# Kernel tuning notes

Measured on AMD Instinct MI355X. Metric: run time of the kernel, lower is better.

## Reference

```python
import jax, jax.numpy as jnp
import numpy as np

N_EMB = 8192
EMB_DIM = 128
BETA = 0.25


def setup_inputs() -> dict:
    key = jax.random.key(0)
    k1, k2 = jax.random.split(key)
    x = jax.random.normal(k1, (32, EMB_DIM, 1024), dtype=jnp.float32)
    embeddings = jax.random.normal(k2, (N_EMB, EMB_DIM), dtype=jnp.float32)
    return {"x": x, "embeddings": embeddings}


def reference(x, embeddings):
    # preprocess: swap chn_dim(=1) with last dim, flatten to tokens
    xt = jnp.swapaxes(x, 1, -1)                      # [B, L, D]
    flat = xt.reshape(-1, EMB_DIM)                   # [N, D]
    prenorm = jnp.linalg.norm(flat - jnp.mean(flat)) / np.sqrt(float(flat.size))

    # squared-euclidean distances via matmul + norms: [N, n_emb]
    s1 = jnp.sum(flat * flat, axis=1, keepdims=True)
    s2 = jnp.sum(embeddings * embeddings, axis=1)
    sim = flat @ embeddings.T
    distances = s1 + s2 - 2.0 * sim

    min_distance = jnp.min(distances, axis=1)
    idx = jnp.argmin(distances, axis=1)              # [N] int
    fit = jnp.mean(jnp.nan_to_num(min_distance))

    # EMA scatter statistics (one-hot matmul in torch == segment_sum here)
    k_sum = jax.ops.segment_sum(flat, idx, num_segments=N_EMB)         # [n_emb, D]
    k_elem = jax.ops.segment_sum(jnp.ones_like(idx, jnp.float32), idx,
                                 num_segments=N_EMB)                   # [n_emb]
    k_prob = k_elem / jnp.sum(k_elem)
    entropy = -jnp.sum(k_prob * jnp.log(k_prob + 1e-8))

    # embedding gather, reshape back to channels-first
    quantized = embeddings[idx].reshape(xt.shape)    # [B, L, D]
    quantized = jnp.swapaxes(quantized, 1, -1)       # [B, D, L]

    # ema_update=True -> codebook_loss = 0, only commit loss
    commit_loss = BETA * jnp.mean((jax.lax.stop_gradient(quantized) - x) ** 2)
    loss = commit_loss

    # straight-through estimator
    out = x + jax.lax.stop_gradient(quantized - x)
    return out, quantized, loss, fit, prenorm, entropy, k_sum, k_elem
```

## Files before the change

kernel.cpp:

```cpp
#include <hip/hip_runtime.h>
#include <math.h>
#include <float.h>

#define BB 32
#define DD 128
#define LL 1024
#define NN 32768
#define NE 8192
#define XSZ 4194304
#define OUT_OFF_Q     4194304
#define OUT_OFF_SCAL  8388608
#define OUT_OFF_KSUM  8388612
#define OUT_OFF_KELEM 9437188

typedef unsigned int u32;
typedef unsigned short u16;
typedef int   i32x4 __attribute__((ext_vector_type(4)));
typedef float f32x4 __attribute__((ext_vector_type(4)));

__device__ inline float waveSum(float v){
  #pragma unroll
  for (int o = 32; o > 0; o >>= 1) v += __shfl_down(v, o, 64);
  return v;
}
__device__ inline double waveSumD(double v){
  #pragma unroll
  for (int o = 32; o > 0; o >>= 1) v += __shfl_down(v, o, 64);
  return v;
}

__global__ __launch_bounds__(256) void prep_kernel(const float* __restrict__ e,
    u16* __restrict__ eh8, int* __restrict__ s2seed,
    int* __restrict__ cnt, float* __restrict__ accs)
{
  int t = threadIdx.x;
  if (blockIdx.x < 32) cnt[blockIdx.x * 256 + t] = 0;
  if (blockIdx.x == 32 && t < 16) accs[t] = 0.f;

  int row = blockIdx.x * 4 + (t >> 6);
  int kd  = t & 63;
  float2 ev = *reinterpret_cast<const float2*>(&e[row * DD + kd * 2]);
  int e0 = __float2int_rn(ev.x * 4096.f);
  int e1 = __float2int_rn(ev.y * 4096.f);
  e0 = min(max(e0, -32639), 32639);
  e1 = min(max(e1, -32639), 32639);
  double sq = (double)e0 * (double)e0 + (double)e1 * (double)e1;
  sq = waveSumD(sq);
  if (kd == 0){
    int sd = (int)(sq * (1.0 / 131072.0));
    sd = min(sd, 120000);
    s2seed[row] = -sd;
  }
  int h0 = (e0 + 128) >> 8;
  int h1 = (e1 + 128) >> 8;
  int k = kd * 2;
  int T16 = row >> 4, lr = row & 15;
  int kt2 = k >> 6, lg = (k >> 4) & 3, j = k & 15;
  int du16 = (((T16*2 + kt2) * 1024) + lg*256 + lr*16 + j) >> 1;
  eh8[du16] = (u16)((h0 & 255) | ((h1 & 255) << 8));
}

#define LOADSET(AH0,AH1,SEED,TT) \
  { int T_ = (TT); \
    AH0 = *(const i32x4*)(ehp + (size_t)(T_*2 + 0) * 256); \
    AH1 = *(const i32x4*)(ehp + (size_t)(T_*2 + 1) * 256); \
    SEED = s2s4[T_*4 + sofs]; }

#define MFMA2S(SLOT, CT, AH0,AH1,SEED) \
  SLOT = __builtin_amdgcn_mfma_i32_16x16x64_i8(AH0, Bh[CT][0], SEED, 0,0,0); \
  SLOT = __builtin_amdgcn_mfma_i32_16x16x64_i8(AH1, Bh[CT][1], SLOT, 0,0,0);

#define KEYS1(T1V, CT, JV) \
  { _Pragma("unroll") \
    for (int r = 0; r < 4; ++r){ \
      int key = (int)(((u32)T1V[r] << 13) + (u32)(JV[r])); \
      int k2n; \
      asm("v_med3_i32 %0, %1, %2, %3" \
          : "=v"(k2n) : "v"(key), "v"(k1[CT]), "v"(k2[CT])); \
      k2[CT] = k2n; \
      k1[CT] = max(key, k1[CT]); \
    } }

#define TILE_BODY(AH0,AH1,SEED,JV) \
  MFMA2S(sa, 0, AH0,AH1,SEED) \
  MFMA2S(sb, 1, AH0,AH1,SEED) \
  KEYS1(sa, 0, JV) \
  MFMA2S(sa, 2, AH0,AH1,SEED) \
  KEYS1(sb, 1, JV) \
  MFMA2S(sb, 3, AH0,AH1,SEED) \
  KEYS1(sa, 2, JV) \
  KEYS1(sb, 3, JV)

__global__ __launch_bounds__(256, 4) void argmin_mfma(
    const float* __restrict__ x,
    const u32* __restrict__ eh8,
    const i32x4* __restrict__ s2s4,
    int* __restrict__ idx1o, int* __restrict__ idx2o)
{
  __shared__ int kk1[1024];
  __shared__ int kk2[1024];

  int t  = threadIdx.x;
  int w  = t >> 6;
  int l  = t & 63;
  int lr = l & 15;
  int lg = l >> 4;

  int blk  = blockIdx.x;
  int half = blk >> 9;
  int tb   = blk & 511;
  int hb64 = half * 64;

  int n0 = tb * 64;
  int b  = n0 >> 10;
  int l0 = n0 & 1023;
  const float* xb = x + (size_t)b * (DD * LL);

  i32x4 Bh[4][2];
  #pragma unroll
  for (int ct = 0; ct < 4; ++ct){
    int tok = l0 + ct*16 + lr;
    #pragma unroll
    for (int kt = 0; kt < 2; ++kt){
      #pragma unroll
      for (int dw = 0; dw < 4; ++dw){
        u32 hw = 0;
        #pragma unroll
        for (int bb = 0; bb < 4; ++bb){
          int k = kt*64 + lg*16 + dw*4 + bb;
          int xi = __float2int_rn(xb[(size_t)k * LL + tok] * 4096.f);
          xi = min(max(xi, -32639), 32639);
          int h  = (xi + 128) >> 8;
          hw |= ((u32)h & 255u) << (8*bb);
        }
        Bh[ct][kt][dw] = (int)hw;
      }
    }
  }

  int k1[4], k2[4];
  #pragma unroll
  for (int ct = 0; ct < 4; ++ct){ k1[ct] = (int)0x80000000; k2[ct] = (int)0x80000000; }

  int jvA[4], jvB[4];
  #pragma unroll
  for (int r = 0; r < 4; ++r){
    jvA[r] = 8191 - (hb64*64 + w*16 + lg*4 + r);
    jvB[r] = jvA[r] - 64;
  }

  const u32* ehp = eh8 + (size_t)l * 4;
  int sofs = lg;

  i32x4 Ah0A, Ah1A, seedA;
  i32x4 Ah0B, Ah1B, seedB;
  i32x4 sa, sb;

  LOADSET(Ah0A, Ah1A, seedA, (hb64 + 0)*4 + w)
  LOADSET(Ah0B, Ah1B, seedB, (hb64 + 1)*4 + w)

  for (int it = 0; it < 64; it += 2){
    TILE_BODY(Ah0A, Ah1A, seedA, jvA)
    if (it + 2 < 64){
      LOADSET(Ah0A, Ah1A, seedA, (hb64 + it + 2)*4 + w)
    }
    #pragma unroll
    for (int r = 0; r < 4; ++r) jvA[r] -= 128;

    TILE_BODY(Ah0B, Ah1B, seedB, jvB)
    if (it + 3 < 64){
      LOADSET(Ah0B, Ah1B, seedB, (hb64 + it + 3)*4 + w)
    }
    #pragma unroll
    for (int r = 0; r < 4; ++r) jvB[r] -= 128;
  }

  #pragma unroll
  for (int ct = 0; ct < 4; ++ct){
    int sidx = (ct*16 + lr)*16 + w*4 + lg;
    kk1[sidx] = k1[ct];
    kk2[sidx] = k2[ct];
  }
  __syncthreads();
  if (t < 64){
    int K1 = (int)0x80000000, K2 = (int)0x80000000;
    #pragma unroll 4
    for (int s = 0; s < 16; ++s){
      int a = kk1[t*16 + s], b2 = kk2[t*16 + s];
      int mn = min(a, K1);  K2 = max(mn, K2);  K1 = max(a, K1);
      mn = min(b2, K1);     K2 = max(mn, K2);  K1 = max(b2, K1);
    }
    idx1o[half*NN + n0 + t] = 8191 - (K1 & 8191);
    idx2o[half*NN + n0 + t] = 8191 - (K2 & 8191);
  }
}

__global__ __launch_bounds__(128) void fixup_kernel(const float* __restrict__ x,
    const float* __restrict__ e,
    const int* __restrict__ idx1, const int* __restrict__ idx2,
    int* __restrict__ idxf, int* __restrict__ cnt, float* __restrict__ accs,
    float* __restrict__ out, float* __restrict__ quant)
{
  int n = blockIdx.x * 128 + threadIdx.x;
  int b = n >> 10, l = n & 1023;
  size_t xoff = (size_t)b * (DD * LL) + l;
  const float* xb = x + xoff;
  int js[4];
  js[0] = idx1[n];      js[1] = idx2[n];
  js[2] = idx1[NN + n]; js[3] = idx2[NN + n];
  const float4* er[4];
  #pragma unroll
  for (int i = 0; i < 4; ++i) er[i] = (const float4*)&e[js[i] * DD];

  float s1 = 0.f, sx = 0.f;
  float dt[4] = {0.f,0.f,0.f,0.f}, sq[4] = {0.f,0.f,0.f,0.f};
  #pragma unroll 2
  for (int k4 = 0; k4 < 32; ++k4){
    float xv[4];
    #pragma unroll
    for (int r = 0; r < 4; ++r) xv[r] = xb[(size_t)(k4*4 + r) * LL];
    s1 = fmaf(xv[0],xv[0], fmaf(xv[1],xv[1], fmaf(xv[2],xv[2], fmaf(xv[3],xv[3], s1))));
    sx += xv[0] + xv[1] + xv[2] + xv[3];
    #pragma unroll
    for (int i = 0; i < 4; ++i){
      float4 v = er[i][k4];
      dt[i] = fmaf(xv[0],v.x, fmaf(xv[1],v.y, fmaf(xv[2],v.z, fmaf(xv[3],v.w, dt[i]))));
      sq[i] = fmaf(v.x,v.x, fmaf(v.y,v.y, fmaf(v.z,v.z, fmaf(v.w,v.w, sq[i]))));
    }
  }
  int jw = js[0];
  float dw = s1 + sq[0] - 2.f * dt[0];
  #pragma unroll
  for (int i = 1; i < 4; ++i){
    float di = s1 + sq[i] - 2.f * dt[i];
    if (di < dw || (di == dw && js[i] < jw)) { dw = di; jw = js[i]; }
  }
  idxf[n] = jw;
  atomicAdd(&cnt[jw], 1);

  const float4* ew = (const float4*)&e[jw * DD];
  #pragma unroll 2
  for (int k4 = 0; k4 < 32; ++k4){
    float4 q = ew[k4];
    #pragma unroll
    for (int r = 0; r < 4; ++r){
      size_t o = xoff + (size_t)(k4*4 + r) * LL;
      float qr = (r == 0) ? q.x : (r == 1) ? q.y : (r == 2) ? q.z : q.w;
      out[o]   = qr;
      quant[o] = qr;
    }
  }
  dw = waveSum(dw); s1 = waveSum(s1); sx = waveSum(sx);
  if ((threadIdx.x & 63) == 0){
    atomicAdd(&accs[3], dw);
    atomicAdd(&accs[1], s1);
    atomicAdd(&accs[0], sx);
  }
}

__global__ __launch_bounds__(1024) void prefix_kernel(const int* __restrict__ cnt,
    int* __restrict__ cursor, float* __restrict__ kelem,
    const float* __restrict__ accs, float* __restrict__ scal)
{
  __shared__ int sc[1024];
  __shared__ double er[16];
  int t = threadIdx.x;
  int c[8]; int s = 0;
  #pragma unroll
  for (int i = 0; i < 8; ++i){ c[i] = cnt[t*8 + i]; s += c[i]; }
  sc[t] = s;
  __syncthreads();
  for (int off = 1; off < 1024; off <<= 1){
    int v = sc[t];
    int u = (t >= off) ? sc[t - off] : 0;
    __syncthreads();
    sc[t] = v + u;
    __syncthreads();
  }
  int base = t ? sc[t-1] : 0;
  #pragma unroll
  for (int i = 0; i < 8; ++i){
    cursor[t*8 + i] = base;
    kelem[t*8 + i] = (float)c[i];
    base += c[i];
  }
  double es = 0.0;
  #pragma unroll
  for (int i = 0; i < 8; ++i){
    float p = (float)c[i] * (1.0f / NN);
    es += (double)(p * logf(p + 1e-8f));
  }
  es = waveSumD(es);
  if ((t & 63) == 0) er[t >> 6] = es;
  __syncthreads();
  if (t == 0){
    double ent = 0.0;
    #pragma unroll
    for (int i = 0; i < 16; ++i) ent += er[i];
    ent = -ent;
    float sum = accs[0], sq = accs[1], fitsum = accs[3];
    double mu  = (double)sum / (double)XSZ;
    double var = (double)sq / (double)XSZ - mu * mu;
    if (var < 0) var = 0;
    scal[0] = (float)(0.25 * (double)fitsum / (double)XSZ);
    scal[1] = (float)((double)fitsum / (double)NN);
    scal[2] = (float)sqrt(var);
    scal[3] = (float)ent;
  }
}

__global__ __launch_bounds__(256) void scatter_kernel(const int* __restrict__ idxf,
    int* __restrict__ cursor, int* __restrict__ order, int* __restrict__ jsorted)
{
  int n = blockIdx.x * 256 + threadIdx.x;
  int j = idxf[n];
  int p = atomicAdd(&cursor[j], 1);
  order[p] = n;
  jsorted[p] = j;
}

__global__ __launch_bounds__(256) void transpose_kernel(const float* __restrict__ x,
    float* __restrict__ xT, float* __restrict__ ksum)
{
  __shared__ float tile[64][137];
  int t = threadIdx.x;
  {
    const float4 z = make_float4(0.f,0.f,0.f,0.f);
    float4* kz = (float4*)&ksum[(size_t)blockIdx.x * 2048 + t * 8];
    kz[0] = z; kz[1] = z;
  }
  int b  = blockIdx.x >> 4;
  int l0 = (blockIdx.x & 15) << 6;
  const float* xb = x + (size_t)b * (DD * LL);
  #pragma unroll
  for (int rep = 0; rep < 32; ++rep){
    int idx = rep * 256 + t;
    int d = idx >> 6, ll = idx & 63;
    tile[ll][d] = xb[d * LL + l0 + ll];
  }
  __syncthreads();
  int n0 = (b << 10) + l0;
  #pragma unroll
  for (int rep = 0; rep < 8; ++rep){
    int idx = rep * 256 + t;
    int row = idx >> 5, c4 = idx & 31;
    float4 v;
    v.x = tile[row][c4*4+0]; v.y = tile[row][c4*4+1];
    v.z = tile[row][c4*4+2]; v.w = tile[row][c4*4+3];
    *(float4*)&xT[(size_t)(n0 + row) * DD + c4*4] = v;
  }
}

__global__ __launch_bounds__(256) void ksum_chunk_kernel(const float* __restrict__ xT,
    const int* __restrict__ order, const int* __restrict__ jsorted,
    float* __restrict__ ksum)
{
  int wv = threadIdx.x >> 6, lane = threadIdx.x & 63;
  int chunk = blockIdx.x * 4 + wv;
  int st = chunk * 32;
  int myo = order[st + (lane & 31)];
  int myj = jsorted[st + (lane & 31)];
  float a0 = 0.f, a1 = 0.f;
  bool inside = false;
  #pragma unroll
  for (int k = 0; k < 32; ++k){
    int j = __shfl(myj, k);
    int n = __shfl(myo, k);
    const float* xr = xT + (size_t)n * DD;
    a0 += xr[lane];
    a1 += xr[64 + lane];
    int jn = (k < 31) ? __shfl(myj, k + 1) : -1;
    if (jn != j){
      if (inside && k < 31){
        ksum[j * DD + lane]      = a0;
        ksum[j * DD + 64 + lane] = a1;
      } else {
        atomicAdd(&ksum[j * DD + lane], a0);
        atomicAdd(&ksum[j * DD + 64 + lane], a1);
      }
      a0 = 0.f; a1 = 0.f;
      inside = true;
    }
  }
}

__global__ __launch_bounds__(256) void ksum_kernel(const float* __restrict__ x,
    const int* __restrict__ order, const int* __restrict__ cnt,
    const int* __restrict__ cursor, float* __restrict__ ksum)
{
  int w = threadIdx.x >> 6, lane = threadIdx.x & 63;
  int j = blockIdx.x * 4 + w;
  int c = cnt[j];
  int st = cursor[j] - c;
  float a0 = 0.f, a1 = 0.f;
  for (int k = 0; k < c; ++k){
    int n = order[st + k];
    int b = n >> 10, l = n & 1023;
    const float* xb = x + (size_t)b * (DD * LL) + l;
    a0 += xb[lane * LL];
    a1 += xb[(lane + 64) * LL];
  }
  ksum[j * DD + lane]      = a0;
  ksum[j * DD + 64 + lane] = a1;
}

extern "C" void kernel_launch(void* const* d_in, const int* in_sizes, int n_in,
                              void* d_out, int out_size, void* d_ws, size_t ws_size,
                              hipStream_t stream)
{
  const float* x = (const float*)d_in[0];
  const float* e = (const float*)d_in[1];
  float* out   = (float*)d_out;
  float* quant = out + OUT_OFF_Q;
  float* scal  = out + OUT_OFF_SCAL;
  float* ksum  = out + OUT_OFF_KSUM;
  float* kelem = out + OUT_OFF_KELEM;

  char* wsb = (char*)d_ws;
  u16*   eh8     = (u16*)(wsb);
  int*   s2seed  = (int*)(wsb + 2097152);
  int*   idx1    = (int*)(wsb + 2129920);
  int*   idx2    = (int*)(wsb + 2392064);
  int*   idxf    = (int*)(wsb + 2654208);
  int*   cnt     = (int*)(wsb + 2785280);
  int*   cursor  = (int*)(wsb + 2818048);
  int*   order   = (int*)(wsb + 2850816);
  int*   jsorted = (int*)(wsb + 2981888);
  float* accs    = (float*)(wsb + 3112960);
  float* xT      = (float*)(wsb + 4194304);
  bool useXT = ws_size >= (size_t)(4194304 + 16777216);

  prep_kernel   <<<NE / 4,     256, 0, stream>>>(e, eh8, s2seed, cnt, accs);
  argmin_mfma   <<<1024,       256, 0, stream>>>(x, (const u32*)eh8,
                                                 (const i32x4*)s2seed, idx1, idx2);
  fixup_kernel  <<<NN / 128,   128, 0, stream>>>(x, e, idx1, idx2, idxf, cnt, accs,
                                                 out, quant);
  prefix_kernel <<<1,         1024, 0, stream>>>(cnt, cursor, kelem, accs, scal);
  scatter_kernel<<<NN / 256,   256, 0, stream>>>(idxf, cursor, order, jsorted);
  if (useXT){
    transpose_kernel <<<BB * 16, 256, 0, stream>>>(x, xT, ksum);
    ksum_chunk_kernel<<<NN / 128, 256, 0, stream>>>(xT, order, jsorted, ksum);
  } else {
    ksum_kernel      <<<NE / 4,  256, 0, stream>>>(x, order, cnt, cursor, ksum);
  }
}
```

Baseline: 147.6 us.

## Fuse x transpose into fixup kernel, split its D loop across waves, precompute codebook norms

The fixup kernel now runs 4 waves per 64 tokens. Each wave handles a quarter of the channel dimension, and partial dot products and norms are reduced through shared memory. It also writes the token-major copy of x that the separate transpose kernel used to build, so x is read once less. Codebook squared norms are computed once in prep instead of per candidate in fixup, and ksum zeroing moves into the scatter kernel. The ksum chunk size is halved to 16 to get more parallelism, at the cost of more atomics at chunk boundaries; the strided per-thread float4 xT writes may coalesce poorly.

After: 152.1 us. +3.1%, slower.

```diff
diff --git a/kernel.cpp b/kernel.cpp
--- a/kernel.cpp
+++ b/kernel.cpp
@@ -30,7 +30,7 @@
 }
 
 __global__ __launch_bounds__(256) void prep_kernel(const float* __restrict__ e,
-    u16* __restrict__ eh8, int* __restrict__ s2seed,
+    u16* __restrict__ eh8, int* __restrict__ s2seed, float* __restrict__ s2f,
     int* __restrict__ cnt, float* __restrict__ accs)
 {
   int t = threadIdx.x;
@@ -46,10 +46,13 @@
   e1 = min(max(e1, -32639), 32639);
   double sq = (double)e0 * (double)e0 + (double)e1 * (double)e1;
   sq = waveSumD(sq);
+  float sqf = ev.x * ev.x + ev.y * ev.y;
+  sqf = waveSum(sqf);
   if (kd == 0){
     int sd = (int)(sq * (1.0 / 131072.0));
     sd = min(sd, 120000);
     s2seed[row] = -sd;
+    s2f[row] = sqf;
   }
   int h0 = (e0 + 128) >> 8;
   int h1 = (e1 + 128) >> 8;
@@ -195,66 +198,93 @@
   }
 }
 
-__global__ __launch_bounds__(128) void fixup_kernel(const float* __restrict__ x,
-    const float* __restrict__ e,
+__global__ __launch_bounds__(256) void fixup_kernel(const float* __restrict__ x,
+    const float* __restrict__ e, const float* __restrict__ s2f,
     const int* __restrict__ idx1, const int* __restrict__ idx2,
     int* __restrict__ idxf, int* __restrict__ cnt, float* __restrict__ accs,
-    float* __restrict__ out, float* __restrict__ quant)
-{
-  int n = blockIdx.x * 128 + threadIdx.x;
-  int b = n >> 10, l = n & 1023;
-  size_t xoff = (size_t)b * (DD * LL) + l;
-  const float* xb = x + xoff;
+    float* __restrict__ out, float* __restrict__ quant, float* __restrict__ xT)
+{
+  __shared__ float red[5][4][64];
+  __shared__ int jws[64];
+
+  int t = threadIdx.x;
+  int w = t >> 6, l = t & 63;
+  int n0 = blockIdx.x * 64;
+  int n  = n0 + l;
+  int b  = n0 >> 10;
+  int l0 = n0 & 1023;
+  size_t base = (size_t)b * (DD * LL) + l0 + l;
+  const float* xb = x + base;
+
   int js[4];
   js[0] = idx1[n];      js[1] = idx2[n];
   js[2] = idx1[NN + n]; js[3] = idx2[NN + n];
-  const float4* er[4];
-  #pragma unroll
-  for (int i = 0; i < 4; ++i) er[i] = (const float4*)&e[js[i] * DD];
 
   float s1 = 0.f, sx = 0.f;
-  float dt[4] = {0.f,0.f,0.f,0.f}, sq[4] = {0.f,0.f,0.f,0.f};
-  #pragma unroll 2
-  for (int k4 = 0; k4 < 32; ++k4){
-    float xv[4];
-    #pragma unroll
-    for (int r = 0; r < 4; ++r) xv[r] = xb[(size_t)(k4*4 + r) * LL];
-    s1 = fmaf(xv[0],xv[0], fmaf(xv[1],xv[1], fmaf(xv[2],xv[2], fmaf(xv[3],xv[3], s1))));
-    sx += xv[0] + xv[1] + xv[2] + xv[3];
-    #pragma unroll
-    for (int i = 0; i < 4; ++i){
-      float4 v = er[i][k4];
-      dt[i] = fmaf(xv[0],v.x, fmaf(xv[1],v.y, fmaf(xv[2],v.z, fmaf(xv[3],v.w, dt[i]))));
-      sq[i] = fmaf(v.x,v.x, fmaf(v.y,v.y, fmaf(v.z,v.z, fmaf(v.w,v.w, sq[i]))));
-    }
-  }
-  int jw = js[0];
-  float dw = s1 + sq[0] - 2.f * dt[0];
-  #pragma unroll
-  for (int i = 1; i < 4; ++i){
-    float di = s1 + sq[i] - 2.f * dt[i];
-    if (di < dw || (di == dw && js[i] < jw)) { dw = di; jw = js[i]; }
-  }
-  idxf[n] = jw;
-  atomicAdd(&cnt[jw], 1);
-
-  const float4* ew = (const float4*)&e[jw * DD];
-  #pragma unroll 2
-  for (int k4 = 0; k4 < 32; ++k4){
-    float4 q = ew[k4];
-    #pragma unroll
-    for (int r = 0; r < 4; ++r){
-      size_t o = xoff + (size_t)(k4*4 + r) * LL;
-      float qr = (r == 0) ? q.x : (r == 1) ? q.y : (r == 2) ? q.z : q.w;
-      out[o]   = qr;
-      quant[o] = qr;
-    }
-  }
-  dw = waveSum(dw); s1 = waveSum(s1); sx = waveSum(sx);
-  if ((threadIdx.x & 63) == 0){
-    atomicAdd(&accs[3], dw);
-    atomicAdd(&accs[1], s1);
-    atomicAdd(&accs[0], sx);
+  float dt0 = 0.f, dt1 = 0.f, dt2 = 0.f, dt3 = 0.f;
+  int kbase = w * 32;
+  #pragma unroll
+  for (int k4 = 0; k4 < 8; ++k4){
+    int k = kbase + k4*4;
+    float x0 = xb[(size_t)(k+0) * LL];
+    float x1 = xb[(size_t)(k+1) * LL];
+    float x2 = xb[(size_t)(k+2) * LL];
+    float x3 = xb[(size_t)(k+3) * LL];
+    s1 = fmaf(x0,x0, fmaf(x1,x1, fmaf(x2,x2, fmaf(x3,x3, s1))));
+    sx += x0 + x1 + x2 + x3;
+    if (xT) *(float4*)&xT[(size_t)n * DD + k] = make_float4(x0,x1,x2,x3);
+    float4 v0 = *(const float4*)&e[(size_t)js[0] * DD + k];
+    float4 v1 = *(const float4*)&e[(size_t)js[1] * DD + k];
+    float4 v2 = *(const float4*)&e[(size_t)js[2] * DD + k];
+    float4 v3 = *(const float4*)&e[(size_t)js[3] * DD + k];
+    dt0 = fmaf(x0,v0.x, fmaf(x1,v0.y, fmaf(x2,v0.z, fmaf(x3,v0.w, dt0))));
+    dt1 = fmaf(x0,v1.x, fmaf(x1,v1.y, fmaf(x2,v1.z, fmaf(x3,v1.w, dt1))));
+    dt2 = fmaf(x0,v2.x, fmaf(x1,v2.y, fmaf(x2,v2.z, fmaf(x3,v2.w, dt2))));
+    dt3 = fmaf(x0,v3.x, fmaf(x1,v3.y, fmaf(x2,v3.z, fmaf(x3,v3.w, dt3))));
+  }
+  red[0][w][l] = s1;
+  red[1][w][l] = dt0;  red[2][w][l] = dt1;
+  red[3][w][l] = dt2;  red[4][w][l] = dt3;
+  sx = waveSum(sx);
+  if (l == 0) atomicAdd(&accs[0], sx);
+  __syncthreads();
+
+  if (w == 0){
+    float S1 = red[0][0][l] + red[0][1][l] + red[0][2][l] + red[0][3][l];
+    float D[4];
+    #pragma unroll
+    for (int i = 0; i < 4; ++i)
+      D[i] = red[1+i][0][l] + red[1+i][1][l] + red[1+i][2][l] + red[1+i][3][l];
+    int jw = js[0];
+    float dw = S1 + s2f[js[0]] - 2.f * D[0];
+    #pragma unroll
+    for (int i = 1; i < 4; ++i){
+      float di = S1 + s2f[js[i]] - 2.f * D[i];
+      if (di < dw || (di == dw && js[i] < jw)) { dw = di; jw = js[i]; }
+    }
+    idxf[n] = jw;
+    atomicAdd(&cnt[jw], 1);
+    jws[l] = jw;
+    float S1s = waveSum(S1);
+    float dws = waveSum(dw);
+    if (l == 0){
+      atomicAdd(&accs[1], S1s);
+      atomicAdd(&accs[3], dws);
+    }
+  }
+  __syncthreads();
+
+  int jw = jws[l];
+  float* ob = out   + base;
+  float* qb = quant + base;
+  #pragma unroll
+  for (int k4 = 0; k4 < 8; ++k4){
+    int k = kbase + k4*4;
+    float4 q = *(const float4*)&e[(size_t)jw * DD + k];
+    ob[(size_t)(k+0)*LL] = q.x;  qb[(size_t)(k+0)*LL] = q.x;
+    ob[(size_t)(k+1)*LL] = q.y;  qb[(size_t)(k+1)*LL] = q.y;
+    ob[(size_t)(k+2)*LL] = q.z;  qb[(size_t)(k+2)*LL] = q.z;
+    ob[(size_t)(k+3)*LL] = q.w;  qb[(size_t)(k+3)*LL] = q.w;
   }
 }
 
@@ -310,68 +340,43 @@
 }
 
 __global__ __launch_bounds__(256) void scatter_kernel(const int* __restrict__ idxf,
-    int* __restrict__ cursor, int* __restrict__ order, int* __restrict__ jsorted)
+    int* __restrict__ cursor, int* __restrict__ order, int* __restrict__ jsorted,
+    float* __restrict__ ksum)
 {
   int n = blockIdx.x * 256 + threadIdx.x;
+  {
+    const float4 z = make_float4(0.f,0.f,0.f,0.f);
+    float4* kz = (float4*)&ksum[(size_t)n * 32];
+    #pragma unroll
+    for (int i = 0; i < 8; ++i) kz[i] = z;
+  }
   int j = idxf[n];
   int p = atomicAdd(&cursor[j], 1);
   order[p] = n;
   jsorted[p] = j;
 }
 
-__global__ __launch_bounds__(256) void transpose_kernel(const float* __restrict__ x,
-    float* __restrict__ xT, float* __restrict__ ksum)
-{
-  __shared__ float tile[64][137];
-  int t = threadIdx.x;
-  {
-    const float4 z = make_float4(0.f,0.f,0.f,0.f);
-    float4* kz = (float4*)&ksum[(size_t)blockIdx.x * 2048 + t * 8];
-    kz[0] = z; kz[1] = z;
-  }
-  int b  = blockIdx.x >> 4;
-  int l0 = (blockIdx.x & 15) << 6;
-  const float* xb = x + (size_t)b * (DD * LL);
-  #pragma unroll
-  for (int rep = 0; rep < 32; ++rep){
-    int idx = rep * 256 + t;
-    int d = idx >> 6, ll = idx & 63;
-    tile[ll][d] = xb[d * LL + l0 + ll];
-  }
-  __syncthreads();
-  int n0 = (b << 10) + l0;
-  #pragma unroll
-  for (int rep = 0; rep < 8; ++rep){
-    int idx = rep * 256 + t;
-    int row = idx >> 5, c4 = idx & 31;
-    float4 v;
-    v.x = tile[row][c4*4+0]; v.y = tile[row][c4*4+1];
-    v.z = tile[row][c4*4+2]; v.w = tile[row][c4*4+3];
-    *(float4*)&xT[(size_t)(n0 + row) * DD + c4*4] = v;
-  }
-}
-
 __global__ __launch_bounds__(256) void ksum_chunk_kernel(const float* __restrict__ xT,
     const int* __restrict__ order, const int* __restrict__ jsorted,
     float* __restrict__ ksum)
 {
   int wv = threadIdx.x >> 6, lane = threadIdx.x & 63;
   int chunk = blockIdx.x * 4 + wv;
-  int st = chunk * 32;
-  int myo = order[st + (lane & 31)];
-  int myj = jsorted[st + (lane & 31)];
+  int st = chunk * 16;
+  int myo = order[st + (lane & 15)];
+  int myj = jsorted[st + (lane & 15)];
   float a0 = 0.f, a1 = 0.f;
   bool inside = false;
   #pragma unroll
-  for (int k = 0; k < 32; ++k){
+  for (int k = 0; k < 16; ++k){
     int j = __shfl(myj, k);
     int n = __shfl(myo, k);
     const float* xr = xT + (size_t)n * DD;
     a0 += xr[lane];
     a1 += xr[64 + lane];
-    int jn = (k < 31) ? __shfl(myj, k + 1) : -1;
+    int jn = (k < 15) ? __shfl(myj, k + 1) : -1;
     if (jn != j){
-      if (inside && k < 31){
+      if (inside && k < 15){
         ksum[j * DD + lane]      = a0;
         ksum[j * DD + 64 + lane] = a1;
       } else {
@@ -418,6 +423,7 @@
 
   char* wsb = (char*)d_ws;
   u16*   eh8     = (u16*)(wsb);
+  float* s2f     = (float*)(wsb + 1048576);
   int*   s2seed  = (int*)(wsb + 2097152);
   int*   idx1    = (int*)(wsb + 2129920);
   int*   idx2    = (int*)(wsb + 2392064);
@@ -430,16 +436,16 @@
   float* xT      = (float*)(wsb + 4194304);
   bool useXT = ws_size >= (size_t)(4194304 + 16777216);
 
-  prep_kernel   <<<NE / 4,     256, 0, stream>>>(e, eh8, s2seed, cnt, accs);
+  prep_kernel   <<<NE / 4,     256, 0, stream>>>(e, eh8, s2seed, s2f, cnt, accs);
   argmin_mfma   <<<1024,       256, 0, stream>>>(x, (const u32*)eh8,
                                                  (const i32x4*)s2seed, idx1, idx2);
-  fixup_kernel  <<<NN / 128,   128, 0, stream>>>(x, e, idx1, idx2, idxf, cnt, accs,
-                                                 out, quant);
+  fixup_kernel  <<<NN / 64,    256, 0, stream>>>(x, e, s2f, idx1, idx2, idxf, cnt,
+                                                 accs, out, quant,
+                                                 useXT ? xT : (float*)nullptr);
   prefix_kernel <<<1,         1024, 0, stream>>>(cnt, cursor, kelem, accs, scal);
-  scatter_kernel<<<NN / 256,   256, 0, stream>>>(idxf, cursor, order, jsorted);
+  scatter_kernel<<<NN / 256,   256, 0, stream>>>(idxf, cursor, order, jsorted, ksum);
   if (useXT){
-    transpose_kernel <<<BB * 16, 256, 0, stream>>>(x, xT, ksum);
-    ksum_chunk_kernel<<<NN / 128, 256, 0, stream>>>(xT, order, jsorted, ksum);
+    ksum_chunk_kernel<<<NN / 64, 256, 0, stream>>>(xT, order, jsorted, ksum);
   } else {
     ksum_kernel      <<<NE / 4,  256, 0, stream>>>(x, order, cnt, cursor, ksum);
   }
```
